# Performance work log

Hardware: AMD Instinct MI355X
Metric: run time of the kernel (lower is better)

## Reference

```python
import jax, jax.numpy as jnp
import numpy as np

IN_FEATURES = 4096
OUT_FEATURES = 4096
WBITS = 4
GROUPSIZE = 128
PACK_FACTOR = 32 // WBITS  # 8
MASK = (1 << WBITS) - 1    # 15


def setup_inputs() -> dict:
    key = jax.random.key(0)
    k1, k2, k3, k4, k5 = jax.random.split(key, 5)
    x = jax.random.normal(k1, (4, 2048, IN_FEATURES), dtype=jnp.float32)
    # Packed 4-bit weights: (in_features*wbits//32, out_features) int32 words.
    qweight = jax.random.randint(k2, (IN_FEATURES * WBITS // 32, OUT_FEATURES),
                                 jnp.iinfo(jnp.int32).min, jnp.iinfo(jnp.int32).max,
                                 dtype=jnp.int32)
    num_groups = IN_FEATURES // GROUPSIZE  # 32
    # Packed zero points: (num_groups, out_features*wbits//32) int32 words.
    qzeros = jax.random.randint(k3, (num_groups, OUT_FEATURES * WBITS // 32),
                                jnp.iinfo(jnp.int32).min, jnp.iinfo(jnp.int32).max,
                                dtype=jnp.int32)
    scales = jax.random.uniform(k4, (num_groups, OUT_FEATURES), dtype=jnp.float32,
                                minval=0.001, maxval=0.02)
    bias = jax.random.normal(k5, (OUT_FEATURES,), dtype=jnp.float32)
    return {"x": x, "qweight": qweight, "qzeros": qzeros, "scales": scales, "bias": bias}


def _unpack4(packed, axis_len):
    """Unpack int32 words along a new inner axis of PACK_FACTOR 4-bit nibbles.

    packed: (..., n_words) -> (..., n_words*PACK_FACTOR) int32 in [0, 15].
    """
    shifts = (jnp.arange(PACK_FACTOR, dtype=jnp.int32) * WBITS)
    nib = (packed[..., :, None] >> shifts) & MASK  # (..., n_words, PACK_FACTOR)
    return nib.reshape(*packed.shape[:-1], axis_len)


def reference(x, qweight, qzeros, scales, bias):
    # Unpack weights: qweight is packed along in_features (dim 0).
    # (in/8, 8, out) -> (in, out) int nibbles.
    shifts = (jnp.arange(PACK_FACTOR, dtype=jnp.int32) * WBITS)
    wq = ((qweight[:, None, :] >> shifts[None, :, None]) & MASK)
    wq = wq.reshape(IN_FEATURES, OUT_FEATURES)  # [in, out] int32 in [0,15]
    # Unpack zeros: packed along out_features (dim 1); AutoGPTQ stores zero-1,
    # so add 1 back at dequant time.
    zq = _unpack4(qzeros, OUT_FEATURES) + 1  # [num_groups, out]
    g_idx = jnp.arange(IN_FEATURES, dtype=jnp.int32) // GROUPSIZE  # [in]
    # Per-group affine dequant: W[i,o] = s[g(i),o] * (wq[i,o] - z[g(i),o])
    W = scales[g_idx] * (wq - zq[g_idx]).astype(scales.dtype)  # [in, out]
    # y = x @ W + b  (x: [b, s, in])
    return jnp.einsum('bsi,io->bso', x, W) + bias
```

## Files before the change

### kernel.cpp

```cpp
#include <hip/hip_runtime.h>
#include <hip/hip_bf16.h>
#include <stdint.h>


#define M_TOT 8192
#define N_TOT 4096
#define K_TOT 4096
#define NT    (K_TOT / 64)

using bf16x8 = __attribute__((ext_vector_type(8))) __bf16;
using f32x4  = __attribute__((ext_vector_type(4))) float;

__device__ __forceinline__ unsigned short f2bf(float f) {
  unsigned u = __builtin_bit_cast(unsigned, f);
  u += 0x7fffu + ((u >> 16) & 1u);
  return (unsigned short)(u >> 16);
}

__global__ void cvt_x_kernel(const float* __restrict__ x,
                             unsigned short* __restrict__ xb, int n) {
  int stride = gridDim.x * blockDim.x * 8;
  for (int i = (blockIdx.x * blockDim.x + threadIdx.x) * 8; i < n; i += stride) {
    float4 a = *reinterpret_cast<const float4*>(x + i);
    float4 b = *reinterpret_cast<const float4*>(x + i + 4);
    unsigned short o[8] = {f2bf(a.x), f2bf(a.y), f2bf(a.z), f2bf(a.w),
                           f2bf(b.x), f2bf(b.y), f2bf(b.z), f2bf(b.w)};
    *reinterpret_cast<uint4*>(xb + i) = *reinterpret_cast<const uint4*>(o);
  }
}

__global__ void dequant_wt_kernel(const int* __restrict__ qweight,
                                  const int* __restrict__ qzeros,
                                  const float* __restrict__ scales,
                                  unsigned short* __restrict__ wt) {
  int t = blockIdx.x * blockDim.x + threadIdx.x;
  int nn = t >> 9;
  int kw = t & 511;
  int g  = kw >> 4;
  unsigned w = (unsigned)qweight[kw * N_TOT + nn];
  float s = scales[g * N_TOT + nn];
  unsigned zw = (unsigned)qzeros[g * (N_TOT / 8) + (nn >> 3)];
  float z = (float)(((zw >> ((nn & 7) * 4)) & 15u) + 1u);
  unsigned short o[8];
#pragma unroll
  for (int j = 0; j < 8; ++j) {
    float v = s * ((float)((w >> (4 * j)) & 15u) - z);
    o[j] = f2bf(v);
  }
  *reinterpret_cast<uint4*>(wt + (size_t)nn * K_TOT + kw * 8) =
      *reinterpret_cast<const uint4*>(o);
}

__device__ __forceinline__ void gll16(const unsigned short* g, const unsigned short* l) {
  __builtin_amdgcn_global_load_lds(
      (const __attribute__((address_space(1))) void*)(uintptr_t)g,
      (__attribute__((address_space(3))) void*)(uintptr_t)l, 16, 0, 0);
}

__global__ __launch_bounds__(512, 2) void gemm_hoist_kernel(
    const unsigned short* __restrict__ A,
    const unsigned short* __restrict__ B,
    const float* __restrict__ bias,
    float* __restrict__ C) {
  __shared__ __align__(16) unsigned short As[2 * 256 * 64];
  __shared__ __align__(16) unsigned short Bs[2 * 256 * 64];

  int bid = blockIdx.x;
  int swz = (bid & 7) * 64 + (bid >> 3);
  int bm = swz & 31, bn = swz >> 5;
  int m0 = bm * 256, n0 = bn * 256;

  int t = threadIdx.x;
  int lane = t & 63;
  int wave = t >> 6;
  int wr = wave >> 2, wc = wave & 3;
  int lr = lane & 15, kq = lane >> 4;

  int rowL0 = t >> 3;
  int jlog  = ((t & 7) ^ (rowL0 & 7)) * 8;
  const unsigned short* aG = A + (size_t)(m0 + rowL0) * K_TOT + jlog;
  const unsigned short* bG = B + (size_t)(n0 + rowL0) * K_TOT + jlog;

  unsigned rbA = (unsigned)((wr * 128 + lr) * 128 + ((kq * 16) ^ ((lr & 7) << 4)));
  unsigned rbB = (unsigned)((wc * 64  + lr) * 128 + ((kq * 16) ^ ((lr & 7) << 4)));

  f32x4 acc[8][4] = {};
  bf16x8 av[2][2][2];
  bf16x8 bh[2][4][2];

#define STAGE(matG, ldsArr, tile, h)                                              \
  do {                                                                            \
    const unsigned short* _g = (matG) + (size_t)(h) * 128 * K_TOT +               \
                               (size_t)(tile) * 64;                               \
    const unsigned short* _l = (ldsArr) + ((tile) & 1) * 16384 + (h) * 8192 +     \
                               t * 8;                                             \
    gll16(_g, _l);                                                                \
    gll16(_g + (size_t)64 * K_TOT, _l + 4096);                                    \
  } while (0)

  STAGE(aG, As, 0, 0);
  STAGE(aG, As, 0, 1);
  STAGE(bG, Bs, 0, 0);
  STAGE(bG, Bs, 0, 1);
  STAGE(bG, Bs, 1, 0);
  STAGE(bG, Bs, 1, 1);
  asm volatile("s_waitcnt vmcnt(4)" ::: "memory");
  __builtin_amdgcn_s_barrier();
  __builtin_amdgcn_sched_barrier(0);

  {
    const char* aB0 = (const char*)As;
    const char* bB0 = (const char*)Bs;
#pragma unroll
    for (int n = 0; n < 4; ++n)
#pragma unroll
      for (int s = 0; s < 2; ++s)
        bh[0][n][s] = *(const bf16x8*)(bB0 + ((rbB + n * 2048) ^ (s * 64)));
#pragma unroll
    for (int mm = 0; mm < 2; ++mm)
#pragma unroll
      for (int s = 0; s < 2; ++s)
        av[0][mm][s] = *(const bf16x8*)(aB0 + ((rbA + mm * 2048) ^ (s * 64)));
  }

#pragma unroll 2
  for (int tt = 0; tt < NT; ++tt) {
    const char* aBuf = (const char*)As + (tt & 1) * 32768;

#pragma unroll
    for (int q = 0; q < 4; ++q) {
      __builtin_amdgcn_s_setprio(1);
#pragma unroll
      for (int s = 0; s < 2; ++s)
#pragma unroll
        for (int mm = 0; mm < 2; ++mm)
#pragma unroll
          for (int n = 0; n < 4; ++n)
            acc[2 * q + mm][n] = __builtin_amdgcn_mfma_f32_16x16x32_bf16(
                av[q & 1][mm][s], bh[tt & 1][n][s], acc[2 * q + mm][n], 0, 0, 0);
      __builtin_amdgcn_s_setprio(0);

      if (q == 0 && tt + 1 < NT) {
        STAGE(aG, As, tt + 1, 0);
        STAGE(aG, As, tt + 1, 1);
      }

      if (q < 3) {
#pragma unroll
        for (int mm = 0; mm < 2; ++mm)
#pragma unroll
          for (int s = 0; s < 2; ++s)
            av[(q + 1) & 1][mm][s] = *(const bf16x8*)(
                aBuf + ((rbA + (2 * (q + 1) + mm) * 2048) ^ (s * 64)));
      }

      if (q == 2) {
        asm volatile("s_waitcnt vmcnt(0)" ::: "memory");
        __builtin_amdgcn_s_barrier();
        __builtin_amdgcn_sched_barrier(0);
        if (tt + 1 < NT) {
          const char* aN = (const char*)As + ((tt + 1) & 1) * 32768;
          const char* bN = (const char*)Bs + ((tt + 1) & 1) * 32768;
#pragma unroll
          for (int n = 0; n < 4; ++n)
#pragma unroll
            for (int s = 0; s < 2; ++s)
              bh[(tt + 1) & 1][n][s] =
                  *(const bf16x8*)(bN + ((rbB + n * 2048) ^ (s * 64)));
#pragma unroll
          for (int mm = 0; mm < 2; ++mm)
#pragma unroll
            for (int s = 0; s < 2; ++s)
              av[0][mm][s] = *(const bf16x8*)(aN + ((rbA + mm * 2048) ^ (s * 64)));
        }
      }

      if (q == 3) {
        if (tt + 2 < NT) {
          STAGE(bG, Bs, tt + 2, 0);
          STAGE(bG, Bs, tt + 2, 1);
        }
        __builtin_amdgcn_s_barrier();
      }
    }
  }
#undef STAGE

#pragma unroll
  for (int n = 0; n < 4; ++n) {
    int ncol = n0 + wc * 64 + n * 16 + lr;
    float bz = bias[ncol];
#pragma unroll
    for (int m = 0; m < 8; ++m) {
      int mrow = m0 + wr * 128 + m * 16 + kq * 4;
#pragma unroll
      for (int r = 0; r < 4; ++r)
        C[(size_t)(mrow + r) * N_TOT + ncol] = acc[m][n][r] + bz;
    }
  }
}

extern "C" void kernel_launch(void* const* d_in, const int* in_sizes, int n_in,
                              void* d_out, int out_size, void* d_ws, size_t ws_size,
                              hipStream_t stream) {
  const float* x       = (const float*)d_in[0];
  const int*   qweight = (const int*)d_in[1];
  const int*   qzeros  = (const int*)d_in[2];
  const float* scales  = (const float*)d_in[3];
  const float* bias    = (const float*)d_in[4];
  float* out = (float*)d_out;

  const size_t xb_bytes = (size_t)M_TOT * K_TOT * 2;
  const size_t wt_bytes = (size_t)N_TOT * K_TOT * 2;
  if (ws_size < xb_bytes + wt_bytes) return;

  unsigned short* Xb = (unsigned short*)d_ws;
  unsigned short* Wt = (unsigned short*)((char*)d_ws + xb_bytes);

  cvt_x_kernel<<<2048, 256, 0, stream>>>(x, Xb, M_TOT * K_TOT);
  dequant_wt_kernel<<<(N_TOT * 512) / 256, 256, 0, stream>>>(qweight, qzeros, scales, Wt);

  dim3 grid((M_TOT / 256) * (N_TOT / 256));
  gemm_hoist_kernel<<<grid, 512, 0, stream>>>(Xb, Wt, bias, out);
}
```

Baseline: 280.8 us.

## Merge x conversion and weight dequant into one prep kernel with LDS-staged loads

```diff
diff --git a/kernel.cpp b/kernel.cpp
--- a/kernel.cpp
+++ b/kernel.cpp
@@ -17,38 +17,59 @@
   return (unsigned short)(u >> 16);
 }
 
-__global__ void cvt_x_kernel(const float* __restrict__ x,
-                             unsigned short* __restrict__ xb, int n) {
-  int stride = gridDim.x * blockDim.x * 8;
-  for (int i = (blockIdx.x * blockDim.x + threadIdx.x) * 8; i < n; i += stride) {
-    float4 a = *reinterpret_cast<const float4*>(x + i);
-    float4 b = *reinterpret_cast<const float4*>(x + i + 4);
-    unsigned short o[8] = {f2bf(a.x), f2bf(a.y), f2bf(a.z), f2bf(a.w),
-                           f2bf(b.x), f2bf(b.y), f2bf(b.z), f2bf(b.w)};
-    *reinterpret_cast<uint4*>(xb + i) = *reinterpret_cast<const uint4*>(o);
-  }
-}
-
-__global__ void dequant_wt_kernel(const int* __restrict__ qweight,
-                                  const int* __restrict__ qzeros,
-                                  const float* __restrict__ scales,
-                                  unsigned short* __restrict__ wt) {
-  int t = blockIdx.x * blockDim.x + threadIdx.x;
-  int nn = t >> 9;
-  int kw = t & 511;
-  int g  = kw >> 4;
-  unsigned w = (unsigned)qweight[kw * N_TOT + nn];
-  float s = scales[g * N_TOT + nn];
-  unsigned zw = (unsigned)qzeros[g * (N_TOT / 8) + (nn >> 3)];
-  float z = (float)(((zw >> ((nn & 7) * 4)) & 15u) + 1u);
-  unsigned short o[8];
-#pragma unroll
-  for (int j = 0; j < 8; ++j) {
-    float v = s * ((float)((w >> (4 * j)) & 15u) - z);
-    o[j] = f2bf(v);
-  }
-  *reinterpret_cast<uint4*>(wt + (size_t)nn * K_TOT + kw * 8) =
-      *reinterpret_cast<const uint4*>(o);
+__global__ __launch_bounds__(256) void prep_kernel(
+    const float* __restrict__ x, unsigned short* __restrict__ xb,
+    const int* __restrict__ qweight, const int* __restrict__ qzeros,
+    const float* __restrict__ scales, unsigned short* __restrict__ wt) {
+  __shared__ int      lw[16][65];
+  __shared__ float    lsc[64];
+  __shared__ unsigned lzw[8];
+
+  int bid = blockIdx.x;
+  if (bid < 2048) {
+    const int n = M_TOT * K_TOT;
+    const int stride = 2048 * 256 * 8;
+    for (int i = (bid * 256 + (int)threadIdx.x) * 8; i < n; i += stride) {
+      float4 a = *reinterpret_cast<const float4*>(x + i);
+      float4 b = *reinterpret_cast<const float4*>(x + i + 4);
+      unsigned short o[8] = {f2bf(a.x), f2bf(a.y), f2bf(a.z), f2bf(a.w),
+                             f2bf(b.x), f2bf(b.y), f2bf(b.z), f2bf(b.w)};
+      *reinterpret_cast<uint4*>(xb + i) = *reinterpret_cast<const uint4*>(o);
+    }
+  } else {
+    int db = bid - 2048;
+    int kt = db >> 6, nt = db & 63;
+    int kw0 = kt * 16, nn0 = nt * 64;
+    int tau = threadIdx.x;
+
+    int col = tau & 63, rowb = tau >> 6;
+#pragma unroll
+    for (int r = 0; r < 4; ++r)
+      lw[rowb + r * 4][col] = qweight[(kw0 + rowb + r * 4) * N_TOT + nn0 + col];
+    int g = kt;
+    if (tau < 64) lsc[tau] = scales[g * N_TOT + nn0 + tau];
+    if (tau < 8)  lzw[tau] = (unsigned)qzeros[g * (N_TOT / 8) + (nn0 >> 3) + tau];
+    __syncthreads();
+
+    int kwc = tau & 15, grp = tau >> 4;
+#pragma unroll
+    for (int j = 0; j < 4; ++j) {
+      int nnr = grp * 4 + j;
+      unsigned w = (unsigned)lw[kwc][nnr];
+      float sc = lsc[nnr];
+      unsigned zw = lzw[nnr >> 3];
+      float zs = sc * (float)(((zw >> ((nnr & 7) * 4)) & 15u) + 1u);
+      unsigned short o[8];
+#pragma unroll
+      for (int jj = 0; jj < 8; ++jj) {
+        float v = sc * (float)((w >> (4 * jj)) & 15u) - zs;
+        o[jj] = f2bf(v);
+      }
+      *reinterpret_cast<uint4*>(wt + (size_t)(nn0 + nnr) * K_TOT +
+                                (kw0 + kwc) * 8) =
+          *reinterpret_cast<const uint4*>(o);
+    }
+  }
 }
 
 __device__ __forceinline__ void gll16(const unsigned short* g, const unsigned short* l) {
@@ -217,8 +238,7 @@
   unsigned short* Xb = (unsigned short*)d_ws;
   unsigned short* Wt = (unsigned short*)((char*)d_ws + xb_bytes);
 
-  cvt_x_kernel<<<2048, 256, 0, stream>>>(x, Xb, M_TOT * K_TOT);
-  dequant_wt_kernel<<<(N_TOT * 512) / 256, 256, 0, stream>>>(qweight, qzeros, scales, Wt);
+  prep_kernel<<<4096, 256, 0, stream>>>(x, Xb, qweight, qzeros, scales, Wt);
 
   dim3 grid((M_TOT / 256) * (N_TOT / 256));
   gemm_hoist_kernel<<<grid, 512, 0, stream>>>(Xb, Wt, bias, out);
```

Result: slower. 298.8 us (+6.4%).
